# Kernel tuning notes

Hardware: AMD Instinct MI355X
Metric: run time of the kernel (lower is better)

## Reference

```python
import jax, jax.numpy as jnp
import numpy as np

H = 512      # memory_width
LIN = 128    # linear_width
IO = 1       # io_width
DEPTH = 2
L = 8192     # input_length


def setup_inputs() -> dict:
    key = jax.random.key(0)
    ks = jax.random.split(key, 12)
    s = 0.05  # small init scale
    return {
        "input": jax.random.normal(ks[0], (L, IO), jnp.float32),
        "residual": jnp.zeros((1, 1, H), jnp.float32),
        "memory": jnp.zeros((DEPTH, 1, H), jnp.float32),
        "W_proc": jax.random.normal(ks[1], (LIN, IO), jnp.float32) * s,
        "b_proc": jax.random.normal(ks[2], (LIN,), jnp.float32) * s,
        "W_ih0": jax.random.normal(ks[3], (3 * H, LIN), jnp.float32) * s,
        "W_hh0": jax.random.normal(ks[4], (3 * H, H), jnp.float32) * s,
        "b_ih0": jax.random.normal(ks[5], (3 * H,), jnp.float32) * s,
        "b_hh0": jax.random.normal(ks[6], (3 * H,), jnp.float32) * s,
        "W_ih1": jax.random.normal(ks[7], (3 * H, H), jnp.float32) * s,
        "W_hh1": jax.random.normal(ks[8], (3 * H, H), jnp.float32) * s,
        "b_ih1": jax.random.normal(ks[9], (3 * H,), jnp.float32) * s,
        "b_hh1": jax.random.normal(ks[10], (3 * H,), jnp.float32) * s,
        "input_length": L,
    }


def _gru_cell(x, h, Wi, Wh, bi, bh):
    # torch nn.GRU cell: gates ordered (r, z, n)
    gi = Wi @ x + bi
    gh = Wh @ h + bh
    i_r, i_z, i_n = jnp.split(gi, 3)
    h_r, h_z, h_n = jnp.split(gh, 3)
    r = jax.nn.sigmoid(i_r + h_r)
    z = jax.nn.sigmoid(i_z + h_z)
    n = jnp.tanh(i_n + r * h_n)
    return (1.0 - z) * n + z * h


def reference(input, residual, memory, W_proc, b_proc,
              W_ih0, W_hh0, b_ih0, b_hh0,
              W_ih1, W_hh1, b_ih1, b_hh1, input_length):
    def step(carry, x_t):
        h0, h1, res = carry
        p = W_proc @ x_t + b_proc                      # Linear(io_width -> linear_width)
        h0 = _gru_cell(p, h0, W_ih0, W_hh0, b_ih0, b_hh0)
        h1 = _gru_cell(h0, h1, W_ih1, W_hh1, b_ih1, b_hh1)
        res = jax.nn.sigmoid(res + h1)                 # residual += rnn_out; sigmoid
        return (h0, h1, res), None

    carry0 = (memory[0, 0], memory[1, 0], residual[0, 0])
    (h0, h1, res), _ = jax.lax.scan(step, carry0, input[: input_length - 1])
    residual_out = res[None, None, :]                  # (1,1,H)
    memory_out = jnp.stack([h0, h1])[:, None, :]       # (depth,1,H)
    return residual_out, memory_out
```

## Files before the change

kernel.cpp:

```cpp
#include <hip/hip_runtime.h>
#include <math.h>

#define Hh   512
#define TH   1536
#define LINN 128
typedef unsigned long long ull;
typedef unsigned int u32;

#define WS_A     0
#define WS_CC    6144
#define WS_RING0 16384
#define WS_RING1 49152

__device__ __forceinline__ float sigm(float v) { return 1.f / (1.f + __expf(-v)); }
__device__ __forceinline__ float tanh_fast(float x) { return 2.f / (1.f + __expf(-2.f * x)) - 1.f; }
__device__ __forceinline__ ull  pk(float v, u32 tag) { return ((ull)tag << 32) | (ull)__float_as_uint(v); }
__device__ __forceinline__ ull  ring_ld(const ull* p) {
    return __hip_atomic_load(p, __ATOMIC_RELAXED, __HIP_MEMORY_SCOPE_AGENT);
}
__device__ __forceinline__ void ring_st(ull* p, ull v) {
    __hip_atomic_store(p, v, __ATOMIC_RELAXED, __HIP_MEMORY_SCOPE_AGENT);
}

__global__ void prep(const float* __restrict__ Wih0, const float* __restrict__ Wproc,
                     const float* __restrict__ bproc, const float* __restrict__ bih0,
                     const float* __restrict__ bhh0, float* __restrict__ A,
                     float* __restrict__ CC)
{
    int row = blockIdx.x * 256 + threadIdx.x;
    if (row >= TH) return;
    const float* w = Wih0 + (size_t)row * LINN;
    float a = 0.f, c = 0.f;
    for (int k = 0; k < LINN; ++k) { float wv = w[k]; a = fmaf(wv, Wproc[k], a); c = fmaf(wv, bproc[k], c); }
    c += bih0[row];
    if (row < 2 * Hh) c += bhh0[row];
    A[row] = a; CC[row] = c;
}

__global__ void ringinit(const float* __restrict__ mem, ull* __restrict__ ring0,
                         ull* __restrict__ ring1)
{
    const int t = threadIdx.x;
    for (int slot = 0; slot < 8; ++slot) {
        ring0[slot * Hh + t] = pk(slot == 7 ? mem[t]      : 0.f, 0u);
        ring1[slot * Hh + t] = pk(slot == 7 ? mem[Hh + t] : 0.f, 0u);
    }
}

__launch_bounds__(256, 1)
__global__ void fused(const float* __restrict__ input, const float* __restrict__ resid,
                      const float* __restrict__ Whh0, const float* __restrict__ bhh0,
                      const float* __restrict__ A, const float* __restrict__ CC,
                      const float* __restrict__ Wih1, const float* __restrict__ Whh1,
                      const float* __restrict__ bih1, const float* __restrict__ bhh1,
                      ull* __restrict__ ring0, ull* __restrict__ ring1,
                      float* __restrict__ outp, int T)
{
    __shared__ __align__(16) float smem[13312];
    const int tid = threadIdx.x;
    const int wg  = blockIdx.x;

    if (wg < 64) {
        float* Wl = smem;
        float* hl = smem + 12288;
        const int jl = tid >> 5;
        const int s2 = tid & 31;
        const int jg = wg * 8 + jl;
        for (int i = tid; i < 24 * Hh; i += 256) {
            int lr = i >> 9, k = i & (Hh - 1);
            int g = lr % 3, j = lr / 3;
            Wl[i] = Whh0[(size_t)(g * Hh + wg * 8 + j) * Hh + k];
        }
        const float Ar = A[jg], Az = A[jg + Hh], An = A[jg + 2 * Hh];
        const float Cr = CC[jg], Cz = CC[jg + Hh], Cn = CC[jg + 2 * Hh];
        const float Bn = bhh0[jg + 2 * Hh];
        const float* Wr = &Wl[(jl * 3 + 0) * Hh];
        const float* Wz = &Wl[(jl * 3 + 1) * Hh];
        const float* Wn = &Wl[(jl * 3 + 2) * Hh];
        __syncthreads();

        for (int s = 0; s < T; ++s) {
            const ull* base = ring0 + ((s - 1) & 7) * Hh;
            const u32 tgt = (u32)s;
            ull w0, w1;
            do { w0 = ring_ld(base + tid);       } while ((u32)(w0 >> 32) < tgt);
            do { w1 = ring_ld(base + tid + 256); } while ((u32)(w1 >> 32) < tgt);
            if (tid == 0 && s >= 7) {
                const ull* bp = ring1 + ((s - 7) & 7) * Hh;
                while ((u32)(ring_ld(bp) >> 32) < (u32)(s - 6)) {}
            }
            __syncthreads();
            hl[tid]       = __uint_as_float((u32)w0);
            hl[tid + 256] = __uint_as_float((u32)w1);
            __syncthreads();
            const float x = input[s];
            float ar = 0.f, az = 0.f, an = 0.f;
#pragma unroll
            for (int i = 0; i < 16; ++i) {
                int k = s2 + 32 * i;
                float hk = hl[k];
                ar = fmaf(Wr[k], hk, ar); az = fmaf(Wz[k], hk, az); an = fmaf(Wn[k], hk, an);
            }
#pragma unroll
            for (int o = 16; o > 0; o >>= 1) {
                ar += __shfl_xor(ar, o); az += __shfl_xor(az, o); an += __shfl_xor(an, o);
            }
            if (s2 == 0) {
                float r  = sigm(fmaf(Ar, x, Cr) + ar);
                float z  = sigm(fmaf(Az, x, Cz) + az);
                float n  = tanh_fast(fmaf(An, x, Cn) + r * (an + Bn));
                float hn = (1.f - z) * n + z * hl[jg];
                ring_st(ring0 + (s & 7) * Hh + jg, pk(hn, (u32)(s + 1)));
                if (s == T - 1) outp[Hh + jg] = hn;
            }
        }
    } else {
        float* Wl  = smem;
        float* hl0 = smem + 12288;
        float* hl1 = smem + 12800;
        const int w  = tid >> 6;
        const int l  = tid & 63;
        const int jg = (wg - 64) * 4 + w;
        for (int i = tid; i < 24 * Hh; i += 256) {
            int lr = i >> 9, k = i & (Hh - 1);
            int ww = lr / 6, q = lr % 6;
            int hj = (wg - 64) * 4 + ww;
            const float* src = (q < 3) ? &Wih1[(size_t)(q * Hh + hj) * Hh]
                                       : &Whh1[(size_t)((q - 3) * Hh + hj) * Hh];
            Wl[i] = src[k];
        }
        const float Br = bih1[jg] + bhh1[jg];
        const float Bz = bih1[jg + Hh] + bhh1[jg + Hh];
        const float Bin = bih1[jg + 2 * Hh];
        const float Bhn = bhh1[jg + 2 * Hh];
        const float* Xr = &Wl[(w * 6 + 0) * Hh];
        const float* Xz = &Wl[(w * 6 + 1) * Hh];
        const float* Xn = &Wl[(w * 6 + 2) * Hh];
        const float* Hr = &Wl[(w * 6 + 3) * Hh];
        const float* Hz = &Wl[(w * 6 + 4) * Hh];
        const float* Hn = &Wl[(w * 6 + 5) * Hh];
        float resl = resid[jg];
        __syncthreads();

        for (int u = 0; u < T; ++u) {
            const ull* b0 = ring0 + (u & 7) * Hh;
            const ull* b1 = ring1 + ((u - 1) & 7) * Hh;
            const u32 t0g = (u32)(u + 1), t1g = (u32)u;
            ull a0, a1, c0, c1;
            do { a0 = ring_ld(b0 + tid);       } while ((u32)(a0 >> 32) < t0g);
            do { a1 = ring_ld(b0 + tid + 256); } while ((u32)(a1 >> 32) < t0g);
            do { c0 = ring_ld(b1 + tid);       } while ((u32)(c0 >> 32) < t1g);
            do { c1 = ring_ld(b1 + tid + 256); } while ((u32)(c1 >> 32) < t1g);
            __syncthreads();
            hl0[tid]       = __uint_as_float((u32)a0);
            hl0[tid + 256] = __uint_as_float((u32)a1);
            hl1[tid]       = __uint_as_float((u32)c0);
            hl1[tid + 256] = __uint_as_float((u32)c1);
            __syncthreads();
            float xr = 0.f, xz = 0.f, xn = 0.f, hr = 0.f, hz = 0.f, hq = 0.f;
#pragma unroll
            for (int i = 0; i < 8; ++i) {
                int k = l + 64 * i;
                float h0k = hl0[k], h1k = hl1[k];
                xr = fmaf(Xr[k], h0k, xr); xz = fmaf(Xz[k], h0k, xz); xn = fmaf(Xn[k], h0k, xn);
                hr = fmaf(Hr[k], h1k, hr); hz = fmaf(Hz[k], h1k, hz); hq = fmaf(Hn[k], h1k, hq);
            }
#pragma unroll
            for (int o = 32; o > 0; o >>= 1) {
                xr += __shfl_xor(xr, o); xz += __shfl_xor(xz, o); xn += __shfl_xor(xn, o);
                hr += __shfl_xor(hr, o); hz += __shfl_xor(hz, o); hq += __shfl_xor(hq, o);
            }
            if (l == 0) {
                float r   = sigm(xr + hr + Br);
                float z   = sigm(xz + hz + Bz);
                float n   = tanh_fast(xn + Bin + r * (hq + Bhn));
                float h1n = (1.f - z) * n + z * hl1[jg];
                ring_st(ring1 + (u & 7) * Hh + jg, pk(h1n, (u32)(u + 1)));
                resl = sigm(resl + h1n);
                if (u == T - 1) { outp[jg] = resl; outp[2 * Hh + jg] = h1n; }
            }
        }
    }
}

extern "C" void kernel_launch(void* const* d_in, const int* in_sizes, int n_in,
                              void* d_out, int out_size, void* d_ws, size_t ws_size,
                              hipStream_t stream)
{
    const float* input    = (const float*)d_in[0];
    const float* residual = (const float*)d_in[1];
    const float* memory   = (const float*)d_in[2];
    const float* Wproc    = (const float*)d_in[3];
    const float* bproc    = (const float*)d_in[4];
    const float* Wih0     = (const float*)d_in[5];
    const float* Whh0     = (const float*)d_in[6];
    const float* bih0     = (const float*)d_in[7];
    const float* bhh0     = (const float*)d_in[8];
    const float* Wih1     = (const float*)d_in[9];
    const float* Whh1     = (const float*)d_in[10];
    const float* bih1     = (const float*)d_in[11];
    const float* bhh1     = (const float*)d_in[12];
    const int L = in_sizes[0];
    const int T = L - 1;
    float* out = (float*)d_out;
    char* ws = (char*)d_ws;

    float* A     = (float*)(ws + WS_A);
    float* CC    = (float*)(ws + WS_CC);
    ull*   ring0 = (ull*)(ws + WS_RING0);
    ull*   ring1 = (ull*)(ws + WS_RING1);

    prep<<<dim3((TH + 255) / 256), dim3(256), 0, stream>>>(Wih0, Wproc, bproc, bih0, bhh0, A, CC);
    ringinit<<<dim3(1), dim3(512), 0, stream>>>(memory, ring0, ring1);
    fused<<<dim3(192), dim3(256), 0, stream>>>(input, residual, Whh0, bhh0, A, CC,
                                               Wih1, Whh1, bih1, bhh1,
                                               ring0, ring1, out, T);
}
```

Baseline: 20.03 ms.

## Deepen ring buffers, double-buffer LDS state, and relax inter-layer backpressure polling

```diff
diff --git a/kernel.cpp b/kernel.cpp
--- a/kernel.cpp
+++ b/kernel.cpp
@@ -4,13 +4,14 @@
 #define Hh   512
 #define TH   1536
 #define LINN 128
+#define RD   16
 typedef unsigned long long ull;
 typedef unsigned int u32;
 
 #define WS_A     0
 #define WS_CC    6144
 #define WS_RING0 16384
-#define WS_RING1 49152
+#define WS_RING1 (16384 + Hh * RD * 8)
 
 __device__ __forceinline__ float sigm(float v) { return 1.f / (1.f + __expf(-v)); }
 __device__ __forceinline__ float tanh_fast(float x) { return 2.f / (1.f + __expf(-2.f * x)) - 1.f; }
@@ -41,9 +42,9 @@
                          ull* __restrict__ ring1)
 {
     const int t = threadIdx.x;
-    for (int slot = 0; slot < 8; ++slot) {
-        ring0[slot * Hh + t] = pk(slot == 7 ? mem[t]      : 0.f, 0u);
-        ring1[slot * Hh + t] = pk(slot == 7 ? mem[Hh + t] : 0.f, 0u);
+    for (int slot = 0; slot < RD; ++slot) {
+        ring0[slot * Hh + t] = pk(slot == RD - 1 ? mem[t]      : 0.f, 0u);
+        ring1[slot * Hh + t] = pk(slot == RD - 1 ? mem[Hh + t] : 0.f, 0u);
     }
 }
 
@@ -56,7 +57,7 @@
                       ull* __restrict__ ring0, ull* __restrict__ ring1,
                       float* __restrict__ outp, int T)
 {
-    __shared__ __align__(16) float smem[13312];
+    __shared__ __align__(16) float smem[14336];
     const int tid = threadIdx.x;
     const int wg  = blockIdx.x;
 
@@ -80,25 +81,29 @@
         __syncthreads();
 
         for (int s = 0; s < T; ++s) {
-            const ull* base = ring0 + ((s - 1) & 7) * Hh;
+            const ull* base = ring0 + (size_t)((s - 1) & (RD - 1)) * Hh;
             const u32 tgt = (u32)s;
-            ull w0, w1;
-            do { w0 = ring_ld(base + tid);       } while ((u32)(w0 >> 32) < tgt);
-            do { w1 = ring_ld(base + tid + 256); } while ((u32)(w1 >> 32) < tgt);
-            if (tid == 0 && s >= 7) {
-                const ull* bp = ring1 + ((s - 7) & 7) * Hh;
-                while ((u32)(ring_ld(bp) >> 32) < (u32)(s - 6)) {}
-            }
-            __syncthreads();
-            hl[tid]       = __uint_as_float((u32)w0);
-            hl[tid + 256] = __uint_as_float((u32)w1);
+            ull w0 = ring_ld(base + tid);
+            ull w1 = ring_ld(base + tid + 256);
+            while (((u32)(w0 >> 32) < tgt) | ((u32)(w1 >> 32) < tgt)) {
+                __builtin_amdgcn_s_sleep(1);
+                w0 = ring_ld(base + tid);
+                w1 = ring_ld(base + tid + 256);
+            }
+            if (tid == 0 && s >= 8 && (s & 7) == 0) {
+                const ull* bp = ring1 + (size_t)((s - 8) & (RD - 1)) * Hh;
+                while ((u32)(ring_ld(bp) >> 32) < (u32)(s - 7)) __builtin_amdgcn_s_sleep(1);
+            }
+            float* hb = hl + (s & 1) * Hh;
+            hb[tid]       = __uint_as_float((u32)w0);
+            hb[tid + 256] = __uint_as_float((u32)w1);
             __syncthreads();
             const float x = input[s];
             float ar = 0.f, az = 0.f, an = 0.f;
 #pragma unroll
             for (int i = 0; i < 16; ++i) {
                 int k = s2 + 32 * i;
-                float hk = hl[k];
+                float hk = hb[k];
                 ar = fmaf(Wr[k], hk, ar); az = fmaf(Wz[k], hk, az); an = fmaf(Wn[k], hk, an);
             }
 #pragma unroll
@@ -109,15 +114,15 @@
                 float r  = sigm(fmaf(Ar, x, Cr) + ar);
                 float z  = sigm(fmaf(Az, x, Cz) + az);
                 float n  = tanh_fast(fmaf(An, x, Cn) + r * (an + Bn));
-                float hn = (1.f - z) * n + z * hl[jg];
-                ring_st(ring0 + (s & 7) * Hh + jg, pk(hn, (u32)(s + 1)));
+                float hn = (1.f - z) * n + z * hb[jg];
+                ring_st(ring0 + (size_t)(s & (RD - 1)) * Hh + jg, pk(hn, (u32)(s + 1)));
                 if (s == T - 1) outp[Hh + jg] = hn;
             }
         }
     } else {
         float* Wl  = smem;
         float* hl0 = smem + 12288;
-        float* hl1 = smem + 12800;
+        float* hl1 = smem + 13312;
         const int w  = tid >> 6;
         const int l  = tid & 63;
         const int jg = (wg - 64) * 4 + w;
@@ -143,25 +148,33 @@
         __syncthreads();
 
         for (int u = 0; u < T; ++u) {
-            const ull* b0 = ring0 + (u & 7) * Hh;
-            const ull* b1 = ring1 + ((u - 1) & 7) * Hh;
+            const ull* b0 = ring0 + (size_t)(u & (RD - 1)) * Hh;
+            const ull* b1 = ring1 + (size_t)((u - 1) & (RD - 1)) * Hh;
             const u32 t0g = (u32)(u + 1), t1g = (u32)u;
-            ull a0, a1, c0, c1;
-            do { a0 = ring_ld(b0 + tid);       } while ((u32)(a0 >> 32) < t0g);
-            do { a1 = ring_ld(b0 + tid + 256); } while ((u32)(a1 >> 32) < t0g);
-            do { c0 = ring_ld(b1 + tid);       } while ((u32)(c0 >> 32) < t1g);
-            do { c1 = ring_ld(b1 + tid + 256); } while ((u32)(c1 >> 32) < t1g);
-            __syncthreads();
-            hl0[tid]       = __uint_as_float((u32)a0);
-            hl0[tid + 256] = __uint_as_float((u32)a1);
-            hl1[tid]       = __uint_as_float((u32)c0);
-            hl1[tid + 256] = __uint_as_float((u32)c1);
+            ull a0 = ring_ld(b0 + tid);
+            ull a1 = ring_ld(b0 + tid + 256);
+            ull c0 = ring_ld(b1 + tid);
+            ull c1 = ring_ld(b1 + tid + 256);
+            while (((u32)(a0 >> 32) < t0g) | ((u32)(a1 >> 32) < t0g) |
+                   ((u32)(c0 >> 32) < t1g) | ((u32)(c1 >> 32) < t1g)) {
+                __builtin_amdgcn_s_sleep(1);
+                a0 = ring_ld(b0 + tid);
+                a1 = ring_ld(b0 + tid + 256);
+                c0 = ring_ld(b1 + tid);
+                c1 = ring_ld(b1 + tid + 256);
+            }
+            float* hb0 = hl0 + (u & 1) * Hh;
+            float* hb1 = hl1 + (u & 1) * Hh;
+            hb0[tid]       = __uint_as_float((u32)a0);
+            hb0[tid + 256] = __uint_as_float((u32)a1);
+            hb1[tid]       = __uint_as_float((u32)c0);
+            hb1[tid + 256] = __uint_as_float((u32)c1);
             __syncthreads();
             float xr = 0.f, xz = 0.f, xn = 0.f, hr = 0.f, hz = 0.f, hq = 0.f;
 #pragma unroll
             for (int i = 0; i < 8; ++i) {
                 int k = l + 64 * i;
-                float h0k = hl0[k], h1k = hl1[k];
+                float h0k = hb0[k], h1k = hb1[k];
                 xr = fmaf(Xr[k], h0k, xr); xz = fmaf(Xz[k], h0k, xz); xn = fmaf(Xn[k], h0k, xn);
                 hr = fmaf(Hr[k], h1k, hr); hz = fmaf(Hz[k], h1k, hz); hq = fmaf(Hn[k], h1k, hq);
             }
@@ -174,8 +187,8 @@
                 float r   = sigm(xr + hr + Br);
                 float z   = sigm(xz + hz + Bz);
                 float n   = tanh_fast(xn + Bin + r * (hq + Bhn));
-                float h1n = (1.f - z) * n + z * hl1[jg];
-                ring_st(ring1 + (u & 7) * Hh + jg, pk(h1n, (u32)(u + 1)));
+                float h1n = (1.f - z) * n + z * hb1[jg];
+                ring_st(ring1 + (size_t)(u & (RD - 1)) * Hh + jg, pk(h1n, (u32)(u + 1)));
                 resl = sigm(resl + h1n);
                 if (u == T - 1) { outp[jg] = resl; outp[2 * Hh + jg] = h1n; }
             }
```

Result: slower. 26.69 ms (+33.2%).
